# Kernel tuning notes

Measured on AMD Instinct MI355X. Metric: run time of the kernel, lower is better.

The kernel has to match this reference:

```python
import jax, jax.numpy as jnp
import numpy as np

B, M, N_STYLE, K, F = 4, 8192, 8192, 8, 288


def _graphconv(x, src, dst, W, b, num_nodes):
    # DGL GraphConv, norm='both': h_v = (sum_{u->v} x_u * d_out(u)^-1/2) * d_in(v)^-1/2 @ W + b
    ones = jnp.ones(src.shape[0], x.dtype)
    deg_out = jnp.clip(jax.ops.segment_sum(ones, src, num_segments=num_nodes), 1.0)
    deg_in = jnp.clip(jax.ops.segment_sum(ones, dst, num_segments=num_nodes), 1.0)
    h = x * (deg_out ** -0.5)[:, None]                      # [N, F] src-normalized
    agg = jax.ops.segment_sum(h[src], dst, num_segments=num_nodes)  # gather+scatter-add
    agg = agg * (deg_in ** -0.5)[:, None]
    return agg @ W + b


def setup_inputs() -> dict:
    key = jax.random.key(0)
    ks = jax.random.split(key, 8)
    return {
        "feat_c": jax.random.normal(ks[0], (B, M, F), jnp.float32),
        "feat_s": jax.random.normal(ks[1], (B, N_STYLE, F), jnp.float32),
        "idx_k1": jax.random.randint(ks[2], (B, M, K), 0, N_STYLE, dtype=jnp.int32),
        "idx_k2": jax.random.randint(ks[3], (B, M, K), 0, M, dtype=jnp.int32),
        "W1": jax.random.normal(ks[4], (F, F), jnp.float32) * (1.0 / np.sqrt(F)),
        "b1": jnp.zeros((F,), jnp.float32),
        "W2": jax.random.normal(ks[5], (F, F), jnp.float32) * (1.0 / np.sqrt(F)),
        "b2": jnp.zeros((F,), jnp.float32),
    }


def reference(feat_c, feat_s, idx_k1, idx_k2, W1, b1, W2, b2):
    b, m, f = feat_c.shape
    n = feat_s.shape[1]
    k = idx_k1.shape[2]
    num_nodes = m + n
    # idx_v: range(m).view(1,m,1).expand(2,m,k).view(-1)
    idx_v = jnp.tile(jnp.repeat(jnp.arange(m, dtype=jnp.int32), k), 2)  # [2*m*k]
    # idx_u: cat((idx_k2, idx_k1 + m), dim=1).view(b, -1)
    idx_u = jnp.concatenate([idx_k2, idx_k1 + m], axis=1).reshape(b, -1)  # [b, 2*m*k]
    feat = jnp.concatenate([feat_c, feat_s], axis=1)  # [b, m+n, f]

    def per_graph(x, src):
        h = _graphconv(x, src, idx_v, W1, b1, num_nodes)
        h = jax.nn.relu(h)
        h = _graphconv(h, src, idx_v, W2, b2, num_nodes)
        return h[:m]  # [m, f]

    return jax.vmap(per_graph)(feat, idx_u)  # [b, m, f]
```

## Files before the change

### kernel.cpp

```cpp
#include <hip/hip_runtime.h>

#define B 4
#define M 8192
#define NSTY 8192
#define KNB 8
#define F 288
#define NT (M + NSTY)
#define BM (B * M)
#define SEGL (M * F)

typedef __attribute__((ext_vector_type(8))) short short8;
typedef __attribute__((ext_vector_type(4))) float floatx4;
typedef __attribute__((ext_vector_type(2))) float floatx2;

__device__ __forceinline__ float u2f(unsigned int u) {
    union { unsigned int u; float f; } c; c.u = u; return c.f;
}
__device__ __forceinline__ unsigned short f2b(float x) {
    union { float f; unsigned int u; } c; c.f = x;
    unsigned int r = c.u + 0x7FFFu + ((c.u >> 16) & 1u);
    return (unsigned short)(r >> 16);
}
__device__ __forceinline__ floatx2 bpair(unsigned int p) {
    floatx2 r;
    r.x = u2f(p << 16);
    r.y = u2f(p & 0xFFFF0000u);
    return r;
}
__device__ __forceinline__ void gload_lds16(const void* g, void* l) {
    __builtin_amdgcn_global_load_lds(
        (const __attribute__((address_space(1))) unsigned int*)g,
        (__attribute__((address_space(3))) unsigned int*)l, 16, 0, 0);
}

#define PREP_CVT   9216
#define PREP_DEG   1024
#define PREP_PKW   648
__global__ void prep_kernel(const int* __restrict__ idx_k1, const int* __restrict__ idx_k2,
                            int* __restrict__ deg,
                            const float* __restrict__ fc, const float* __restrict__ fs,
                            unsigned short* __restrict__ fb,
                            const float* __restrict__ W1, const float* __restrict__ W2,
                            unsigned short* __restrict__ Wp1, unsigned short* __restrict__ Wp2) {
    int blk = blockIdx.x;
    if (blk < PREP_CVT) {
        int seg = blk / 1152;
        int bis = blk - seg * 1152;
        int b = seg >> 1, sty = seg & 1;
        unsigned int e = (unsigned int)bis * 2048 + threadIdx.x * 8;
        const float* src = (sty ? fs : fc) + (size_t)b * SEGL + e;
        float4 x0 = *(const float4*)src;
        float4 x1 = *(const float4*)(src + 4);
        uint4 o;
        o.x = (unsigned int)f2b(x0.x) | ((unsigned int)f2b(x0.y) << 16);
        o.y = (unsigned int)f2b(x0.z) | ((unsigned int)f2b(x0.w) << 16);
        o.z = (unsigned int)f2b(x1.x) | ((unsigned int)f2b(x1.y) << 16);
        o.w = (unsigned int)f2b(x1.z) | ((unsigned int)f2b(x1.w) << 16);
        *(uint4*)(fb + (size_t)b * 2 * SEGL + (size_t)sty * SEGL + e) = o;
    } else if (blk < PREP_CVT + PREP_DEG) {
        int t = (blk - PREP_CVT) * 256 + threadIdx.x;
        int b = t >> 16;
        atomicAdd(&deg[b * NT + idx_k2[t]], 1);
        atomicAdd(&deg[b * NT + M + idx_k1[t]], 1);
    } else {
        int t = (blk - PREP_CVT - PREP_DEG) * 256 + threadIdx.x;
        if (t >= 2 * F * F) return;
        int half = t >= F * F;
        int tt = t - half * F * F;
        int k = tt / F, n = tt - k * F;
        const float* W = half ? W2 : W1;
        unsigned short* Wp = half ? Wp2 : Wp1;
        Wp[((size_t)(k >> 3) * F + n) * 8 + (k & 7)] = f2b(W[tt]);
    }
}

template<int LAYER>
__global__ __launch_bounds__(256) void agg_kernel(
        const unsigned short* __restrict__ src_tbl,
        const int* __restrict__ idx_k1, const int* __restrict__ idx_k2,
        const int* __restrict__ deg, const float* __restrict__ b1,
        unsigned short* __restrict__ aggb) {
    const int NK = (LAYER == 1) ? 16 : 8;
    int tid = threadIdx.x, wid = tid >> 6, lane = tid & 63;
    int blk = blockIdx.x;
    int rx = blk & 7;
    int b = rx >> 1;
    int sub = (blk >> 3) * 2 + (rx & 1);
    int rbase = sub * 16 + wid * 4;

    int i4 = lane >> 4, e = lane & 15;
    size_t eb = ((size_t)b * M + rbase + i4) * KNB;
    int u;
    if (e < 8) u = idx_k2[eb + e];
    else       u = M + idx_k1[eb + e - 8];
    int dg = deg[b * NT + u];
    float w = rsqrtf((float)(dg < 1 ? 1 : dg));
    float wst = (e >= 8) ? w : 0.f;

    float bb[8];
    if (LAYER == 2 && lane < 36) {
        float4 t0 = *(const float4*)(b1 + 8 * lane);
        float4 t1 = *(const float4*)(b1 + 8 * lane + 4);
        bb[0]=fmaxf(t0.x,0.f); bb[1]=fmaxf(t0.y,0.f); bb[2]=fmaxf(t0.z,0.f); bb[3]=fmaxf(t0.w,0.f);
        bb[4]=fmaxf(t1.x,0.f); bb[5]=fmaxf(t1.y,0.f); bb[6]=fmaxf(t1.z,0.f); bb[7]=fmaxf(t1.w,0.f);
    }

    const unsigned short* base = src_tbl + (size_t)b * (LAYER == 1 ? NT : M) * F;
    unsigned short* dbase = aggb + ((size_t)b * M + rbase) * F;

    #pragma unroll
    for (int i = 0; i < 4; ++i) {
        floatx2 acc[4];
        if (LAYER == 2) {
            float S = 0.f;
            #pragma unroll
            for (int j = 8; j < 16; ++j) S += __shfl(wst, i * 16 + j);
            #pragma unroll
            for (int j = 0; j < 4; ++j) { acc[j].x = bb[2*j] * S; acc[j].y = bb[2*j+1] * S; }
        } else {
            #pragma unroll
            for (int j = 0; j < 4; ++j) acc[j] = (floatx2){0.f, 0.f};
        }

        #pragma unroll
        for (int c = 0; c < NK / 8; ++c) {
            const unsigned short* sp[8];
            #pragma unroll
            for (int k = 0; k < 8; ++k) {
                int uk = __shfl(u, i * 16 + c * 8 + k);
                sp[k] = base + (size_t)uk * F + 8 * lane;
            }
            uint4 v[8];
            if (lane < 36) {
                #pragma unroll
                for (int k = 0; k < 8; ++k) v[k] = *(const uint4*)sp[k];
            }
            #pragma unroll
            for (int k = 0; k < 8; ++k) {
                float wk = __shfl(w, i * 16 + c * 8 + k);
                floatx2 wk2 = {wk, wk};
                acc[0] += wk2 * bpair(v[k].x);
                acc[1] += wk2 * bpair(v[k].y);
                acc[2] += wk2 * bpair(v[k].z);
                acc[3] += wk2 * bpair(v[k].w);
            }
        }

        if (lane < 36) {
            uint4 o;
            o.x = (unsigned int)f2b(acc[0].x*0.25f) | ((unsigned int)f2b(acc[0].y*0.25f) << 16);
            o.y = (unsigned int)f2b(acc[1].x*0.25f) | ((unsigned int)f2b(acc[1].y*0.25f) << 16);
            o.z = (unsigned int)f2b(acc[2].x*0.25f) | ((unsigned int)f2b(acc[2].y*0.25f) << 16);
            o.w = (unsigned int)f2b(acc[3].x*0.25f) | ((unsigned int)f2b(acc[3].y*0.25f) << 16);
            *(uint4*)(dbase + (size_t)i * F + 8 * lane) = o;
        }
    }
}

template<int RELU, int OUTBF16>
__global__ __launch_bounds__(256, 2) void gemm_kernel(
        const unsigned short* __restrict__ A,
        const unsigned short* __restrict__ Wp,
        const float* __restrict__ bias,
        void* __restrict__ Cout) {
    __shared__ __align__(16) unsigned short sA[64 * F];
    __shared__ __align__(16) unsigned short sB[2][4 * F * 8];
    int tid = threadIdx.x;
    int wid = tid >> 6, lane = tid & 63;
    int wm = wid & 1, wn = wid >> 1;
    int quad = lane >> 4, r16 = lane & 15;
    int blk = blockIdx.x;
    int rx = blk & 7;
    int b = rx >> 1;
    int sub = (blk >> 3) * 2 + (rx & 1);
    int row0 = b * M + sub * 64;

    const unsigned short* Ab = A + (size_t)row0 * F;
    #pragma unroll
    for (int rr = 0; rr < 9; ++rr)
        gload_lds16(Ab + (rr * 256 + tid) * 8, &sA[(rr * 256 + tid) * 8]);
    if (tid < 128) {
        #pragma unroll
        for (int rr = 0; rr < 9; ++rr)
            gload_lds16(Wp + (rr * 128 + tid) * 8, &sB[0][(rr * 128 + tid) * 8]);
    }

    floatx4 acc[9][2];
    #pragma unroll
    for (int ct = 0; ct < 9; ++ct)
        #pragma unroll
        for (int rt = 0; rt < 2; ++rt)
            acc[ct][rt] = (floatx4){0.f, 0.f, 0.f, 0.f};

    __syncthreads();

    for (int s = 0; s < 9; ++s) {
        if (s < 8 && tid < 128) {
            const unsigned short* src = Wp + (size_t)(s + 1) * 4 * F * 8;
            unsigned short* dstb = sB[(s + 1) & 1];
            #pragma unroll
            for (int rr = 0; rr < 9; ++rr)
                gload_lds16(src + (rr * 128 + tid) * 8, dstb + (rr * 128 + tid) * 8);
        }
        short8 a0 = *(const short8*)&sA[(wm * 32 + r16) * F + s * 32 + quad * 8];
        short8 a1 = *(const short8*)&sA[(wm * 32 + 16 + r16) * F + s * 32 + quad * 8];
        const unsigned short* bbp = &sB[s & 1][(quad * F + wn * 144 + r16) * 8];
        #pragma unroll
        for (int ct = 0; ct < 9; ++ct) {
            short8 bf = *(const short8*)(bbp + ct * 128);
            acc[ct][0] = __builtin_amdgcn_mfma_f32_16x16x32_bf16(a0, bf, acc[ct][0], 0, 0, 0);
            acc[ct][1] = __builtin_amdgcn_mfma_f32_16x16x32_bf16(a1, bf, acc[ct][1], 0, 0, 0);
        }
        __syncthreads();
    }

    #pragma unroll
    for (int ct = 0; ct < 9; ++ct) {
        int col = wn * 144 + ct * 16 + r16;
        float bc = bias[col];
        #pragma unroll
        for (int rt = 0; rt < 2; ++rt) {
            #pragma unroll
            for (int rg = 0; rg < 4; ++rg) {
                float v = acc[ct][rt][rg] + bc;
                if (RELU) v = fmaxf(v, 0.f);
                int grow = row0 + wm * 32 + quad * 4 + rt * 16 + rg;
                if (OUTBF16) ((unsigned short*)Cout)[(size_t)grow * F + col] = f2b(v);
                else         ((float*)Cout)[(size_t)grow * F + col] = v;
            }
        }
    }
}

extern "C" void kernel_launch(void* const* d_in, const int* in_sizes, int n_in,
                              void* d_out, int out_size, void* d_ws, size_t ws_size,
                              hipStream_t stream) {
    const float* feat_c = (const float*)d_in[0];
    const float* feat_s = (const float*)d_in[1];
    const int*   idx_k1 = (const int*)d_in[2];
    const int*   idx_k2 = (const int*)d_in[3];
    const float* W1     = (const float*)d_in[4];
    const float* b1     = (const float*)d_in[5];
    const float* W2     = (const float*)d_in[6];
    const float* b2     = (const float*)d_in[7];

    char* ws = (char*)d_ws;
    int*            deg  = (int*)ws;
    unsigned short* Wp1  = (unsigned short*)(ws + 262144);
    unsigned short* Wp2  = (unsigned short*)(ws + 262144 + 165888);
    unsigned short* aggb = (unsigned short*)(ws + 262144 + 2 * 165888);

    unsigned short* featb = (unsigned short*)d_out;
    unsigned short* h1b   = (unsigned short*)d_out;
    float*          out   = (float*)d_out;

    hipMemsetAsync(deg, 0, (size_t)B * NT * sizeof(int), stream);
    prep_kernel<<<PREP_CVT + PREP_DEG + PREP_PKW, 256, 0, stream>>>(
        idx_k1, idx_k2, deg, feat_c, feat_s, featb, W1, W2, Wp1, Wp2);

    agg_kernel<1><<<BM / 16, 256, 0, stream>>>(featb, idx_k1, idx_k2, deg, b1, aggb);
    gemm_kernel<1, 1><<<BM / 64, 256, 0, stream>>>(aggb, Wp1, b1, (void*)h1b);

    agg_kernel<2><<<BM / 16, 256, 0, stream>>>(h1b, idx_k1, idx_k2, deg, b1, aggb);
    gemm_kernel<0, 0><<<BM / 64, 256, 0, stream>>>(aggb, Wp2, b2, (void*)out);
}
```

Measured before the change: 229.8 us.

## Fuse neighbor aggregation into GEMM kernel via LDS-resident aggregated tile

Merges each layer's gather-aggregate kernel with its following GEMM. Each 64-row block now aggregates its rows straight into shared memory and runs the MFMA GEMM on that tile, so the bf16 aggregate no longer makes a round trip through global memory and two launches are dropped. Weight fragments are read directly from global memory (L2-cached) instead of being double-buffered in LDS. h1 moves from d_out to the workspace. The prep conversion also processes 16 elements per thread instead of 8. The trade-off is fewer blocks (BM/64), which lowers the parallelism available to the latency-bound gather.

```diff
diff --git a/kernel.cpp b/kernel.cpp
--- a/kernel.cpp
+++ b/kernel.cpp
@@ -27,13 +27,8 @@
     r.y = u2f(p & 0xFFFF0000u);
     return r;
 }
-__device__ __forceinline__ void gload_lds16(const void* g, void* l) {
-    __builtin_amdgcn_global_load_lds(
-        (const __attribute__((address_space(1))) unsigned int*)g,
-        (__attribute__((address_space(3))) unsigned int*)l, 16, 0, 0);
-}
-
-#define PREP_CVT   9216
+
+#define PREP_CVT   4608
 #define PREP_DEG   1024
 #define PREP_PKW   648
 __global__ void prep_kernel(const int* __restrict__ idx_k1, const int* __restrict__ idx_k2,
@@ -44,19 +39,27 @@
                             unsigned short* __restrict__ Wp1, unsigned short* __restrict__ Wp2) {
     int blk = blockIdx.x;
     if (blk < PREP_CVT) {
-        int seg = blk / 1152;
-        int bis = blk - seg * 1152;
+        int seg = blk / 576;
+        int bis = blk - seg * 576;
         int b = seg >> 1, sty = seg & 1;
-        unsigned int e = (unsigned int)bis * 2048 + threadIdx.x * 8;
+        unsigned int e = (unsigned int)bis * 4096 + threadIdx.x * 16;
         const float* src = (sty ? fs : fc) + (size_t)b * SEGL + e;
         float4 x0 = *(const float4*)src;
         float4 x1 = *(const float4*)(src + 4);
-        uint4 o;
-        o.x = (unsigned int)f2b(x0.x) | ((unsigned int)f2b(x0.y) << 16);
-        o.y = (unsigned int)f2b(x0.z) | ((unsigned int)f2b(x0.w) << 16);
-        o.z = (unsigned int)f2b(x1.x) | ((unsigned int)f2b(x1.y) << 16);
-        o.w = (unsigned int)f2b(x1.z) | ((unsigned int)f2b(x1.w) << 16);
-        *(uint4*)(fb + (size_t)b * 2 * SEGL + (size_t)sty * SEGL + e) = o;
+        float4 x2 = *(const float4*)(src + 8);
+        float4 x3 = *(const float4*)(src + 12);
+        uint4 o0, o1;
+        o0.x = (unsigned int)f2b(x0.x) | ((unsigned int)f2b(x0.y) << 16);
+        o0.y = (unsigned int)f2b(x0.z) | ((unsigned int)f2b(x0.w) << 16);
+        o0.z = (unsigned int)f2b(x1.x) | ((unsigned int)f2b(x1.y) << 16);
+        o0.w = (unsigned int)f2b(x1.z) | ((unsigned int)f2b(x1.w) << 16);
+        o1.x = (unsigned int)f2b(x2.x) | ((unsigned int)f2b(x2.y) << 16);
+        o1.y = (unsigned int)f2b(x2.z) | ((unsigned int)f2b(x2.w) << 16);
+        o1.z = (unsigned int)f2b(x3.x) | ((unsigned int)f2b(x3.y) << 16);
+        o1.w = (unsigned int)f2b(x3.z) | ((unsigned int)f2b(x3.w) << 16);
+        unsigned short* d = fb + (size_t)b * 2 * SEGL + (size_t)sty * SEGL + e;
+        *(uint4*)d = o0;
+        *(uint4*)(d + 8) = o1;
     } else if (blk < PREP_CVT + PREP_DEG) {
         int t = (blk - PREP_CVT) * 256 + threadIdx.x;
         int b = t >> 16;
@@ -75,28 +78,22 @@
 }
 
 template<int LAYER>
-__global__ __launch_bounds__(256) void agg_kernel(
+__global__ __launch_bounds__(256, 4) void fused_kernel(
         const unsigned short* __restrict__ src_tbl,
         const int* __restrict__ idx_k1, const int* __restrict__ idx_k2,
         const int* __restrict__ deg, const float* __restrict__ b1,
-        unsigned short* __restrict__ aggb) {
+        const unsigned short* __restrict__ Wp, const float* __restrict__ bias,
+        void* __restrict__ Cout) {
+    __shared__ __align__(16) unsigned short sA[64 * F];
     const int NK = (LAYER == 1) ? 16 : 8;
     int tid = threadIdx.x, wid = tid >> 6, lane = tid & 63;
     int blk = blockIdx.x;
     int rx = blk & 7;
     int b = rx >> 1;
     int sub = (blk >> 3) * 2 + (rx & 1);
-    int rbase = sub * 16 + wid * 4;
+    int row0 = b * M + sub * 64;
 
     int i4 = lane >> 4, e = lane & 15;
-    size_t eb = ((size_t)b * M + rbase + i4) * KNB;
-    int u;
-    if (e < 8) u = idx_k2[eb + e];
-    else       u = M + idx_k1[eb + e - 8];
-    int dg = deg[b * NT + u];
-    float w = rsqrtf((float)(dg < 1 ? 1 : dg));
-    float wst = (e >= 8) ? w : 0.f;
-
     float bb[8];
     if (LAYER == 2 && lane < 36) {
         float4 t0 = *(const float4*)(b1 + 8 * lane);
@@ -104,87 +101,68 @@
         bb[0]=fmaxf(t0.x,0.f); bb[1]=fmaxf(t0.y,0.f); bb[2]=fmaxf(t0.z,0.f); bb[3]=fmaxf(t0.w,0.f);
         bb[4]=fmaxf(t1.x,0.f); bb[5]=fmaxf(t1.y,0.f); bb[6]=fmaxf(t1.z,0.f); bb[7]=fmaxf(t1.w,0.f);
     }
-
     const unsigned short* base = src_tbl + (size_t)b * (LAYER == 1 ? NT : M) * F;
-    unsigned short* dbase = aggb + ((size_t)b * M + rbase) * F;
-
-    #pragma unroll
-    for (int i = 0; i < 4; ++i) {
-        floatx2 acc[4];
-        if (LAYER == 2) {
-            float S = 0.f;
+
+    for (int g = 0; g < 4; ++g) {
+        int lr0 = wid * 16 + g * 4;
+        size_t eb = ((size_t)row0 + lr0 + i4) * KNB;
+        int u;
+        if (e < 8) u = idx_k2[eb + e];
+        else       u = M + idx_k1[eb + e - 8];
+        int dg = deg[b * NT + u];
+        float w = rsqrtf((float)(dg < 1 ? 1 : dg));
+        float wst = (e >= 8) ? w : 0.f;
+
+        #pragma unroll
+        for (int i = 0; i < 4; ++i) {
+            floatx2 acc[4];
+            if (LAYER == 2) {
+                float S = 0.f;
+                #pragma unroll
+                for (int j = 8; j < 16; ++j) S += __shfl(wst, i * 16 + j);
+                #pragma unroll
+                for (int j = 0; j < 4; ++j) { acc[j].x = bb[2*j] * S; acc[j].y = bb[2*j+1] * S; }
+            } else {
+                #pragma unroll
+                for (int j = 0; j < 4; ++j) acc[j] = (floatx2){0.f, 0.f};
+            }
             #pragma unroll
-            for (int j = 8; j < 16; ++j) S += __shfl(wst, i * 16 + j);
-            #pragma unroll
-            for (int j = 0; j < 4; ++j) { acc[j].x = bb[2*j] * S; acc[j].y = bb[2*j+1] * S; }
-        } else {
-            #pragma unroll
-            for (int j = 0; j < 4; ++j) acc[j] = (floatx2){0.f, 0.f};
+            for (int c = 0; c < NK / 8; ++c) {
+                const unsigned short* sp[8];
+                #pragma unroll
+                for (int k = 0; k < 8; ++k) {
+                    int uk = __shfl(u, i * 16 + c * 8 + k);
+                    sp[k] = base + (size_t)uk * F + 8 * lane;
+                }
+                uint4 v[8];
+                if (lane < 36) {
+                    #pragma unroll
+                    for (int k = 0; k < 8; ++k) v[k] = *(const uint4*)sp[k];
+                }
+                #pragma unroll
+                for (int k = 0; k < 8; ++k) {
+                    float wk = __shfl(w, i * 16 + c * 8 + k);
+                    floatx2 wk2 = {wk, wk};
+                    acc[0] += wk2 * bpair(v[k].x);
+                    acc[1] += wk2 * bpair(v[k].y);
+                    acc[2] += wk2 * bpair(v[k].z);
+                    acc[3] += wk2 * bpair(v[k].w);
+                }
+            }
+            if (lane < 36) {
+                uint4 o;
+                o.x = (unsigned int)f2b(acc[0].x*0.25f) | ((unsigned int)f2b(acc[0].y*0.25f) << 16);
+                o.y = (unsigned int)f2b(acc[1].x*0.25f) | ((unsigned int)f2b(acc[1].y*0.25f) << 16);
+                o.z = (unsigned int)f2b(acc[2].x*0.25f) | ((unsigned int)f2b(acc[2].y*0.25f) << 16);
+                o.w = (unsigned int)f2b(acc[3].x*0.25f) | ((unsigned int)f2b(acc[3].y*0.25f) << 16);
+                *(uint4*)(&sA[(lr0 + i) * F] + 8 * lane) = o;
+            }
         }
-
-        #pragma unroll
-        for (int c = 0; c < NK / 8; ++c) {
-            const unsigned short* sp[8];
-            #pragma unroll
-            for (int k = 0; k < 8; ++k) {
-                int uk = __shfl(u, i * 16 + c * 8 + k);
-                sp[k] = base + (size_t)uk * F + 8 * lane;
-            }
-            uint4 v[8];
-            if (lane < 36) {
-                #pragma unroll
-                for (int k = 0; k < 8; ++k) v[k] = *(const uint4*)sp[k];
-            }
-            #pragma unroll
-            for (int k = 0; k < 8; ++k) {
-                float wk = __shfl(w, i * 16 + c * 8 + k);
-                floatx2 wk2 = {wk, wk};
-                acc[0] += wk2 * bpair(v[k].x);
-                acc[1] += wk2 * bpair(v[k].y);
-                acc[2] += wk2 * bpair(v[k].z);
-                acc[3] += wk2 * bpair(v[k].w);
-            }
-        }
-
-        if (lane < 36) {
-            uint4 o;
-            o.x = (unsigned int)f2b(acc[0].x*0.25f) | ((unsigned int)f2b(acc[0].y*0.25f) << 16);
-            o.y = (unsigned int)f2b(acc[1].x*0.25f) | ((unsigned int)f2b(acc[1].y*0.25f) << 16);
-            o.z = (unsigned int)f2b(acc[2].x*0.25f) | ((unsigned int)f2b(acc[2].y*0.25f) << 16);
-            o.w = (unsigned int)f2b(acc[3].x*0.25f) | ((unsigned int)f2b(acc[3].y*0.25f) << 16);
-            *(uint4*)(dbase + (size_t)i * F + 8 * lane) = o;
-        }
-    }
-}
-
-template<int RELU, int OUTBF16>
-__global__ __launch_bounds__(256, 2) void gemm_kernel(
-        const unsigned short* __restrict__ A,
-        const unsigned short* __restrict__ Wp,
-        const float* __restrict__ bias,
-        void* __restrict__ Cout) {
-    __shared__ __align__(16) unsigned short sA[64 * F];
-    __shared__ __align__(16) unsigned short sB[2][4 * F * 8];
-    int tid = threadIdx.x;
-    int wid = tid >> 6, lane = tid & 63;
+    }
+    __syncthreads();
+
     int wm = wid & 1, wn = wid >> 1;
     int quad = lane >> 4, r16 = lane & 15;
-    int blk = blockIdx.x;
-    int rx = blk & 7;
-    int b = rx >> 1;
-    int sub = (blk >> 3) * 2 + (rx & 1);
-    int row0 = b * M + sub * 64;
-
-    const unsigned short* Ab = A + (size_t)row0 * F;
-    #pragma unroll
-    for (int rr = 0; rr < 9; ++rr)
-        gload_lds16(Ab + (rr * 256 + tid) * 8, &sA[(rr * 256 + tid) * 8]);
-    if (tid < 128) {
-        #pragma unroll
-        for (int rr = 0; rr < 9; ++rr)
-            gload_lds16(Wp + (rr * 128 + tid) * 8, &sB[0][(rr * 128 + tid) * 8]);
-    }
-
     floatx4 acc[9][2];
     #pragma unroll
     for (int ct = 0; ct < 9; ++ct)
@@ -192,26 +170,16 @@
         for (int rt = 0; rt < 2; ++rt)
             acc[ct][rt] = (floatx4){0.f, 0.f, 0.f, 0.f};
 
-    __syncthreads();
-
     for (int s = 0; s < 9; ++s) {
-        if (s < 8 && tid < 128) {
-            const unsigned short* src = Wp + (size_t)(s + 1) * 4 * F * 8;
-            unsigned short* dstb = sB[(s + 1) & 1];
-            #pragma unroll
-            for (int rr = 0; rr < 9; ++rr)
-                gload_lds16(src + (rr * 128 + tid) * 8, dstb + (rr * 128 + tid) * 8);
-        }
         short8 a0 = *(const short8*)&sA[(wm * 32 + r16) * F + s * 32 + quad * 8];
         short8 a1 = *(const short8*)&sA[(wm * 32 + 16 + r16) * F + s * 32 + quad * 8];
-        const unsigned short* bbp = &sB[s & 1][(quad * F + wn * 144 + r16) * 8];
+        const unsigned short* bp = Wp + ((size_t)(s * 4 + quad) * F + wn * 144 + r16) * 8;
         #pragma unroll
         for (int ct = 0; ct < 9; ++ct) {
-            short8 bf = *(const short8*)(bbp + ct * 128);
+            short8 bf = *(const short8*)(bp + ct * 128);
             acc[ct][0] = __builtin_amdgcn_mfma_f32_16x16x32_bf16(a0, bf, acc[ct][0], 0, 0, 0);
             acc[ct][1] = __builtin_amdgcn_mfma_f32_16x16x32_bf16(a1, bf, acc[ct][1], 0, 0, 0);
         }
-        __syncthreads();
     }
 
     #pragma unroll
@@ -223,10 +191,11 @@
             #pragma unroll
             for (int rg = 0; rg < 4; ++rg) {
                 float v = acc[ct][rt][rg] + bc;
-                if (RELU) v = fmaxf(v, 0.f);
                 int grow = row0 + wm * 32 + quad * 4 + rt * 16 + rg;
-                if (OUTBF16) ((unsigned short*)Cout)[(size_t)grow * F + col] = f2b(v);
-                else         ((float*)Cout)[(size_t)grow * F + col] = v;
+                if (LAYER == 1)
+                    ((unsigned short*)Cout)[(size_t)grow * F + col] = f2b(fmaxf(v, 0.f));
+                else
+                    ((float*)Cout)[(size_t)grow * F + col] = v;
             }
         }
     }
@@ -248,19 +217,14 @@
     int*            deg  = (int*)ws;
     unsigned short* Wp1  = (unsigned short*)(ws + 262144);
     unsigned short* Wp2  = (unsigned short*)(ws + 262144 + 165888);
-    unsigned short* aggb = (unsigned short*)(ws + 262144 + 2 * 165888);
-
+    unsigned short* h1b  = (unsigned short*)(ws + 262144 + 2 * 165888);
     unsigned short* featb = (unsigned short*)d_out;
-    unsigned short* h1b   = (unsigned short*)d_out;
     float*          out   = (float*)d_out;
 
     hipMemsetAsync(deg, 0, (size_t)B * NT * sizeof(int), stream);
     prep_kernel<<<PREP_CVT + PREP_DEG + PREP_PKW, 256, 0, stream>>>(
         idx_k1, idx_k2, deg, feat_c, feat_s, featb, W1, W2, Wp1, Wp2);
 
-    agg_kernel<1><<<BM / 16, 256, 0, stream>>>(featb, idx_k1, idx_k2, deg, b1, aggb);
-    gemm_kernel<1, 1><<<BM / 64, 256, 0, stream>>>(aggb, Wp1, b1, (void*)h1b);
-
-    agg_kernel<2><<<BM / 16, 256, 0, stream>>>(h1b, idx_k1, idx_k2, deg, b1, aggb);
-    gemm_kernel<0, 0><<<BM / 64, 256, 0, stream>>>(aggb, Wp2, b2, (void*)out);
-}
+    fused_kernel<1><<<BM / 64, 256, 0, stream>>>(featb, idx_k1, idx_k2, deg, b1, Wp1, b1, (void*)h1b);
+    fused_kernel<2><<<BM / 64, 256, 0, stream>>>(h1b,   idx_k1, idx_k2, deg, b1, Wp2, b2, (void*)out);
+}
```

After: 502.6 us. 2.19x slower.
